# Kernel optimization log

Measured on AMD Instinct MI355X. Metric: run time of the kernel, lower is better.

The kernel has to match this reference:

```python
import jax, jax.numpy as jnp
import numpy as np

N, C, H, W = 4, 256, 64, 64
E = C // 2  # embed_dim = max(C//2, 1)


def setup_inputs() -> dict:
    key = jax.random.key(0)
    k1, k2, k3, k4 = jax.random.split(key, 4)
    x = jax.random.normal(k1, (N, C, H, W), dtype=jnp.float32)
    # 1x1 conv weights == channel-mixing matrices (bias=False), std=0.01 init
    W_theta = jax.random.normal(k2, (E, C), dtype=jnp.float32) * 0.01
    W_phi = jax.random.normal(k3, (E, C), dtype=jnp.float32) * 0.01
    W_proj = jax.random.normal(k4, (C, C), dtype=jnp.float32) * 0.01  # zero_init=False
    return {"x": x, "W_theta": W_theta, "W_phi": W_phi, "W_proj": W_proj}


def reference(x, W_theta, W_phi, W_proj):
    n, c, h, w = x.shape
    s = h * w
    xf = x.reshape(n, c, s)                      # [N, C, S]
    theta = jnp.einsum('ec,ncs->nes', W_theta, xf)  # [N, E, S]
    phi = jnp.einsum('ec,ncs->nes', W_phi, xf)      # [N, E, S]
    # f = theta^T @ phi, scaled by sqrt(embed_dim) (theta.shape[-1] after permute)
    scale = jnp.sqrt(jnp.asarray(theta.shape[1], dtype=x.dtype))
    f = jnp.einsum('nes,net->nst', theta, phi) / scale  # [N, S, S]
    f = jax.nn.softmax(f, axis=-1)
    # y = f @ g^T with g = x (unembedded values)
    y = jnp.einsum('nst,nct->ncs', f, xf)        # [N, C, S]
    residual = jnp.einsum('oc,ncs->nos', W_proj, y).reshape(n, c, h, w)
    return x + residual
```

## Files before the change

### kernel.cpp

```cpp
#include <hip/hip_runtime.h>
#include <cmath>

#define C_DIM 256
#define E_DIM 128
#define S_DIM 4096

typedef __bf16 bf16x8 __attribute__((ext_vector_type(8)));
typedef float  f32x4  __attribute__((ext_vector_type(4)));
typedef short  s16x8  __attribute__((ext_vector_type(8)));
typedef short  s16x4  __attribute__((ext_vector_type(4)));

__device__ __forceinline__ unsigned short f2bf(float f) {
  union { float f; unsigned u; } v; v.f = f;
  unsigned r = v.u + 0x7FFFu + ((v.u >> 16) & 1u);
  return (unsigned short)(r >> 16);
}
__device__ __forceinline__ unsigned short f2bf_tr(float f) {
  union { float f; unsigned u; } v; v.f = f;
  return (unsigned short)(v.u >> 16);
}
__device__ __forceinline__ bf16x8 as_bf(s16x8 v) {
  union { s16x8 s; bf16x8 b; } u; u.s = v; return u.b;
}
__device__ __forceinline__ bf16x8 f2b8(f32x4 v) { union { f32x4 f; bf16x8 b; } u; u.f = v; return u.b; }
__device__ __forceinline__ f32x4 b2f8(bf16x8 v) { union { bf16x8 b; f32x4 f; } u; u.b = v; return u.f; }
__device__ __forceinline__ f32x4 s2f8(s16x8 v)  { union { s16x8 s; f32x4 f; } u; u.s = v; return u.f; }
__device__ __forceinline__ s16x8 f2s8(f32x4 v)  { union { f32x4 f; s16x8 s; } u; u.f = v; return u.s; }

__global__ __launch_bounds__(256) void cast_w_kernel(
    const float* __restrict__ Wth, const float* __restrict__ Wph,
    const float* __restrict__ Wpr, short* __restrict__ Wb) {
  int t = blockIdx.x * 256 + threadIdx.x;
  int i = t * 4;
  const float* src; int j;
  if (i < 32768)      { src = Wth; j = i; }
  else if (i < 65536) { src = Wph; j = i - 32768; }
  else                { src = Wpr; j = i - 65536; }
  float4 v = *(const float4*)(src + j);
  s16x4 o;
  o[0] = (short)f2bf(v.x); o[1] = (short)f2bf(v.y);
  o[2] = (short)f2bf(v.z); o[3] = (short)f2bf(v.w);
  *(s16x4*)(Wb + i) = o;
}

__global__ __launch_bounds__(256) void mix_kernel(
    const float* __restrict__ x, const short* __restrict__ Wb,
    short* __restrict__ Qg, short* __restrict__ Kg, short* __restrict__ Xb,
    float qscale) {
  __shared__ short lxT[32 * C_DIM];
  int bid = blockIdx.x;
  int n = bid >> 7, s0 = (bid & 127) * 32;
  int tid = threadIdx.x;
  int wid = tid >> 6, lane = tid & 63, l15 = lane & 15, l4 = lane >> 4;

  {
    int cp = tid >> 1, su = tid & 1;
    const float* r0 = x + ((size_t)n * C_DIM + 2 * cp) * S_DIM + s0 + su * 16;
    const float* r1 = r0 + S_DIM;
    float a0[16], a1[16];
    #pragma unroll
    for (int j = 0; j < 4; ++j) {
      *(float4*)(a0 + 4 * j) = *(const float4*)(r0 + 4 * j);
      *(float4*)(a1 + 4 * j) = *(const float4*)(r1 + 4 * j);
    }
    short b0[16], b1[16];
    #pragma unroll
    for (int j = 0; j < 16; ++j) { b0[j] = (short)f2bf(a0[j]); b1[j] = (short)f2bf(a1[j]); }
    short* xb0 = Xb + ((size_t)n * C_DIM + 2 * cp) * S_DIM + s0 + su * 16;
    *(s16x8*)(xb0)             = *(s16x8*)(b0);
    *(s16x8*)(xb0 + 8)         = *(s16x8*)(b0 + 8);
    *(s16x8*)(xb0 + S_DIM)     = *(s16x8*)(b1);
    *(s16x8*)(xb0 + S_DIM + 8) = *(s16x8*)(b1 + 8);
    #pragma unroll
    for (int j = 0; j < 16; ++j) {
      int s = su * 16 + j;
      unsigned d = (unsigned)(unsigned short)b0[j] |
                   ((unsigned)(unsigned short)b1[j] << 16);
      *(unsigned*)((char*)lxT + s * 512 + ((4 * cp) ^ ((s & 7) << 4))) = d;
    }
  }
  __syncthreads();

  const short* Wq = Wb;
  const short* Wk = Wb + 32768;
  const f32x4 fzero = {0.f, 0.f, 0.f, 0.f};
  f32x4 accQ[2][2], accK[2][2];
  #pragma unroll
  for (int a = 0; a < 2; ++a)
    #pragma unroll
    for (int b = 0; b < 2; ++b) { accQ[a][b] = fzero; accK[a][b] = fzero; }

  #pragma unroll 2
  for (int kk = 0; kk < 8; ++kk) {
    bf16x8 bfr[2];
    #pragma unroll
    for (int nf = 0; nf < 2; ++nf) {
      int s = nf * 16 + l15;
      bfr[nf] = *(const bf16x8*)((char*)lxT + s * 512 +
                                 ((kk * 64 + l4 * 16) ^ ((s & 7) << 4)));
    }
    #pragma unroll
    for (int mf = 0; mf < 2; ++mf) {
      int e = wid * 32 + mf * 16 + l15;
      bf16x8 aq = *(const bf16x8*)(Wq + e * C_DIM + kk * 32 + l4 * 8);
      bf16x8 ak = *(const bf16x8*)(Wk + e * C_DIM + kk * 32 + l4 * 8);
      #pragma unroll
      for (int nf = 0; nf < 2; ++nf) {
        accQ[mf][nf] = __builtin_amdgcn_mfma_f32_16x16x32_bf16(aq, bfr[nf], accQ[mf][nf], 0, 0, 0);
        accK[mf][nf] = __builtin_amdgcn_mfma_f32_16x16x32_bf16(ak, bfr[nf], accK[mf][nf], 0, 0, 0);
      }
    }
  }

  #pragma unroll
  for (int mf = 0; mf < 2; ++mf) {
    #pragma unroll
    for (int nf = 0; nf < 2; ++nf) {
      int e = wid * 32 + mf * 16 + l4 * 4;
      int s = s0 + nf * 16 + l15;
      s16x4 pq, pk;
      #pragma unroll
      for (int r = 0; r < 4; ++r) {
        pq[r] = (short)f2bf(accQ[mf][nf][r] * qscale);
        pk[r] = (short)f2bf(accK[mf][nf][r]);
      }
      *(s16x4*)(Qg + ((size_t)n * S_DIM + s) * E_DIM + e) = pq;
      *(s16x4*)(Kg + ((size_t)n * S_DIM + s) * E_DIM + e) = pk;
    }
  }
}


#define QF(qs, ec) f2b8(RA[(qs) * 4 + (ec)])

#define QKT_BODY(KBUF)                                                        \
  {                                                                           \
    const char* kb = (const char*)lK + (KBUF) * 16384;                        \
    char* pw = (char*)lP + (KBUF) * 8192;                                     \
    RB[0] = fzero; RB[1] = fzero; RB[2] = fzero; RB[3] = fzero;               \
    int trow = tq * 16 + l15;                                                 \
    int swz = (trow & 7) << 4;                                                \
    __builtin_amdgcn_s_setprio(1);                                            \
    _Pragma("unroll")                                                         \
    for (int ec = 0; ec < 4; ++ec) {                                          \
      bf16x8 kf = *(const bf16x8*)(kb + trow * 256 + ((ec * 64 + l4 * 16) ^ swz)); \
      _Pragma("unroll")                                                       \
      for (int qs = 0; qs < 4; ++qs)                                          \
        RB[qs] = __builtin_amdgcn_mfma_f32_16x16x32_bf16(kf, QF(qs, ec), RB[qs], 0, 0, 0); \
    }                                                                         \
    __builtin_amdgcn_s_setprio(0);                                            \
    int tb2 = tq * 32 + l4 * 8;                                               \
    _Pragma("unroll")                                                         \
    for (int qs = 0; qs < 4; ++qs) {                                          \
      float p0 = __builtin_amdgcn_exp2f(RB[qs][0]);                           \
      float p1 = __builtin_amdgcn_exp2f(RB[qs][1]);                           \
      float p2 = __builtin_amdgcn_exp2f(RB[qs][2]);                           \
      float p3 = __builtin_amdgcn_exp2f(RB[qs][3]);                           \
      lsum[qs] += (p0 + p1) + (p2 + p3);                                      \
      uint2 dd;                                                               \
      dd.x = (unsigned)f2bf_tr(p0) | ((unsigned)f2bf_tr(p1) << 16);           \
      dd.y = (unsigned)f2bf_tr(p2) | ((unsigned)f2bf_tr(p3) << 16);           \
      int q = qs * 16 + l15;                                                  \
      *(uint2*)(pw + q * 128 + (tb2 ^ ((q & 7) << 4))) = dd;                  \
    }                                                                         \
  }

#define PV_VISSUE(OFF, TI)                                                    \
  _Pragma("unroll")                                                           \
  for (int kk = 0; kk < 2; ++kk)                                              \
    _Pragma("unroll")                                                         \
    for (int ct = 0; ct < 4; ++ct)                                            \
      RA[(OFF) + kk * 4 + ct] = s2f8(*(const s16x8*)(                         \
          Vb + (size_t)(cq * 64 + ct * 16 + l15) * S_DIM + (TI) * 64 + kk * 32 + l4 * 8));

#define PV_KCOMMIT(OFF, KBUFW)                                                \
  {                                                                           \
    char* kw = (char*)lK + (KBUFW) * 16384;                                   \
    _Pragma("unroll")                                                         \
    for (int jj = 0; jj < 4; ++jj) {                                          \
      int r = kr + 16 * jj;                                                   \
      *(s16x8*)(kw + r * 256 + ((kc * 16) ^ ((r & 7) << 4))) = f2s8(RB[(OFF) + jj]); \
    }                                                                         \
  }

#define PV_KLOAD(OFF, TI)                                                     \
  _Pragma("unroll")                                                           \
  for (int jj = 0; jj < 4; ++jj)                                              \
    RB[(OFF) + jj] = s2f8(*(const s16x8*)(                                    \
        Kb + (size_t)((TI) * 64 + kr + 16 * jj) * E_DIM + kc * 8));

#define PV_MFMA(OFF, PBUF)                                                    \
  {                                                                           \
    const char* pr = (const char*)lP + (PBUF) * 8192;                         \
    _Pragma("unroll")                                                         \
    for (int kk = 0; kk < 2; ++kk) {                                          \
      bf16x8 pf[4];                                                           \
      _Pragma("unroll")                                                       \
      for (int qs = 0; qs < 4; ++qs) {                                        \
        int q = qs * 16 + l15;                                                \
        pf[qs] = *(const bf16x8*)(pr + q * 128 + ((kk * 64 + l4 * 16) ^ ((q & 7) << 4))); \
      }                                                                       \
      __builtin_amdgcn_s_setprio(1);                                          \
      _Pragma("unroll")                                                       \
      for (int ct = 0; ct < 4; ++ct) {                                        \
        bf16x8 vf = as_bf(f2s8(RA[(OFF) + kk * 4 + ct]));                     \
        _Pragma("unroll")                                                     \
        for (int qs = 0; qs < 4; ++qs)                                        \
          acc[qs][ct] = __builtin_amdgcn_mfma_f32_16x16x32_bf16(pf[qs], vf, acc[qs][ct], 0, 0, 0); \
      }                                                                       \
      __builtin_amdgcn_s_setprio(0);                                          \
    }                                                                         \
  }

#define RAW_BARRIER()                                                         \
  asm volatile("s_waitcnt lgkmcnt(0)" ::: "memory");                          \
  __builtin_amdgcn_s_barrier();

__global__ __launch_bounds__(512, 2) void attn_kernel(
    const short* __restrict__ Qg, const short* __restrict__ Kg,
    const short* __restrict__ Xb, short* __restrict__ Yg) {
  __shared__ short lK[2 * 64 * E_DIM];
  __shared__ short lP[2 * 64 * 64];
  __shared__ float lsred[4 * 64];

  int bid = blockIdx.x;
  int xcd = bid & 7;
  int n   = xcd >> 1;
  int s0  = (((xcd & 1) << 5) + (bid >> 3)) * 64;

  int tid = threadIdx.x;
  int wid = tid >> 6, lane = tid & 63;
  int l15 = lane & 15, l4 = lane >> 4;

  const short* Kb = Kg + (size_t)n * S_DIM * E_DIM;
  const short* Vb = Xb + (size_t)n * (size_t)C_DIM * S_DIM;

  const f32x4 fzero = {0.f, 0.f, 0.f, 0.f};

  f32x4 RA[16];
  f32x4 RB[8];
  float lsum[4];
  f32x4 acc[4][4];

  int tq = wid;
  int cq = wid - 4;
  int idx = tid & 255;
  int kr = idx >> 4, kc = idx & 15;

  if (wid < 4) {
    #pragma unroll
    for (int qs = 0; qs < 4; ++qs) {
      const short* qp = Qg + ((size_t)n * S_DIM + s0 + qs * 16 + l15) * E_DIM + l4 * 8;
      #pragma unroll
      for (int ec = 0; ec < 4; ++ec) RA[qs * 4 + ec] = b2f8(*(const bf16x8*)(qp + ec * 32));
    }
    #pragma unroll
    for (int j = 0; j < 4; ++j) lsum[j] = 0.f;
  } else {
    #pragma unroll
    for (int a = 0; a < 4; ++a)
      #pragma unroll
      for (int b = 0; b < 4; ++b) acc[a][b] = fzero;
    PV_KLOAD(0, 0);
    PV_KCOMMIT(0, 0);
    PV_KLOAD(4, 1);
    PV_VISSUE(0, 0);
  }
  RAW_BARRIER();

  for (int j = 0; j < 32; ++j) {
    int i0 = 2 * j;
    if (wid < 4) {
      QKT_BODY(0);
    } else {
      if (j > 0)  PV_VISSUE(0, i0);
      PV_KCOMMIT(4, 1);
      if (j > 0)  PV_MFMA(8, 1);
      if (j < 31) PV_KLOAD(0, i0 + 2);
    }
    RAW_BARRIER();
    if (wid < 4) {
      QKT_BODY(1);
    } else {
      PV_VISSUE(8, i0 + 1);
      if (j < 31) PV_KCOMMIT(0, 0);
      PV_MFMA(0, 0);
      if (j < 31) PV_KLOAD(4, i0 + 3);
    }
    RAW_BARRIER();
  }
  if (wid >= 4) {
    PV_MFMA(8, 1);
  }

  if (wid < 4) {
    #pragma unroll
    for (int qs = 0; qs < 4; ++qs) {
      float v = lsum[qs];
      v += __shfl_xor(v, 16);
      v += __shfl_xor(v, 32);
      if (lane < 16) lsred[tq * 64 + qs * 16 + l15] = v;
    }
  }
  __syncthreads();

  short* yst = lK;
  if (wid >= 4) {
    #pragma unroll
    for (int qs = 0; qs < 4; ++qs) {
      #pragma unroll
      for (int r = 0; r < 4; ++r) {
        int q = qs * 16 + l4 * 4 + r;
        float tot = lsred[q] + lsred[64 + q] + lsred[128 + q] + lsred[192 + q];
        float rl = 1.0f / tot;
        #pragma unroll
        for (int ct = 0; ct < 4; ++ct) {
          int c = cq * 64 + ct * 16 + l15;
          *(unsigned short*)((char*)yst + q * 512 + ((c * 2) ^ ((q & 7) << 4))) =
              f2bf_tr(acc[qs][ct][r] * rl);
        }
      }
    }
  }
  __syncthreads();

  int rr = tid >> 3, chb = tid & 7;
  #pragma unroll
  for (int it = 0; it < 4; ++it) {
    int ch = chb + 8 * it;
    s16x8 v = *(const s16x8*)((char*)yst + rr * 512 + ((ch * 16) ^ ((rr & 7) << 4)));
    *(s16x8*)(Yg + ((size_t)n * S_DIM + s0 + rr) * C_DIM + ch * 8) = v;
  }
}

__global__ __launch_bounds__(256) void proj_kernel(
    const short* __restrict__ Yg, const short* __restrict__ Wpb,
    const float* __restrict__ x, float* __restrict__ out) {
  int bid = blockIdx.x;
  int n = bid >> 7, s0 = (bid & 127) * 32;
  int tid = threadIdx.x;
  int wid = tid >> 6, lane = tid & 63, l15 = lane & 15, l4 = lane >> 4;

  const f32x4 fzero = {0.f, 0.f, 0.f, 0.f};
  f32x4 acc[2][4];
  #pragma unroll
  for (int a = 0; a < 2; ++a)
    #pragma unroll
    for (int b = 0; b < 4; ++b) acc[a][b] = fzero;

  const short* ybase = Yg + (size_t)n * S_DIM * C_DIM;

  #pragma unroll 2
  for (int kk = 0; kk < 8; ++kk) {
    bf16x8 af[2];
    #pragma unroll
    for (int mf = 0; mf < 2; ++mf)
      af[mf] = *(const bf16x8*)(ybase + (size_t)(s0 + mf * 16 + l15) * C_DIM +
                                kk * 32 + l4 * 8);
    #pragma unroll
    for (int nf = 0; nf < 4; ++nf) {
      int o = wid * 64 + nf * 16 + l15;
      bf16x8 bfr = *(const bf16x8*)(Wpb + o * C_DIM + kk * 32 + l4 * 8);
      #pragma unroll
      for (int mf = 0; mf < 2; ++mf)
        acc[mf][nf] = __builtin_amdgcn_mfma_f32_16x16x32_bf16(af[mf], bfr, acc[mf][nf], 0, 0, 0);
    }
  }

  #pragma unroll
  for (int mf = 0; mf < 2; ++mf) {
    #pragma unroll
    for (int nf = 0; nf < 4; ++nf) {
      int o = wid * 64 + nf * 16 + l15;
      size_t idx = ((size_t)n * C_DIM + o) * (size_t)S_DIM + s0 + mf * 16 + l4 * 4;
      float4 xv = *(const float4*)(x + idx);
      float4 r;
      r.x = xv.x + acc[mf][nf][0];
      r.y = xv.y + acc[mf][nf][1];
      r.z = xv.z + acc[mf][nf][2];
      r.w = xv.w + acc[mf][nf][3];
      *(float4*)(out + idx) = r;
    }
  }
}

extern "C" void kernel_launch(void* const* d_in, const int* in_sizes, int n_in,
                              void* d_out, int out_size, void* d_ws, size_t ws_size,
                              hipStream_t stream) {
  const float* x   = (const float*)d_in[0];
  const float* Wth = (const float*)d_in[1];
  const float* Wph = (const float*)d_in[2];
  const float* Wpr = (const float*)d_in[3];
  float* out = (float*)d_out;

  short* q_ws  = (short*)d_ws;
  short* k_ws  = q_ws  + (size_t)4 * S_DIM * E_DIM;
  short* xb_ws = k_ws  + (size_t)4 * S_DIM * E_DIM;
  short* y_ws  = xb_ws + (size_t)4 * C_DIM * S_DIM;
  short* wb_ws = y_ws  + (size_t)4 * S_DIM * C_DIM;

  float qscale = 1.4426950408889634f / sqrtf(128.0f);

  cast_w_kernel<<<128, 256, 0, stream>>>(Wth, Wph, Wpr, wb_ws);
  mix_kernel<<<512, 256, 0, stream>>>(x, wb_ws, q_ws, k_ws, xb_ws, qscale);
  attn_kernel<<<256, 512, 0, stream>>>(q_ws, k_ws, xb_ws, y_ws);
  proj_kernel<<<512, 256, 0, stream>>>(y_ws, wb_ws + 65536, x, out);
}
```

Baseline: 115.6 us.

## Split attention key range across two blocks and enlarge query tile to 128

```diff
diff --git a/kernel.cpp b/kernel.cpp
--- a/kernel.cpp
+++ b/kernel.cpp
@@ -18,6 +18,10 @@
 __device__ __forceinline__ unsigned short f2bf_tr(float f) {
   union { float f; unsigned u; } v; v.f = f;
   return (unsigned short)(v.u >> 16);
+}
+__device__ __forceinline__ float bf2f(unsigned short b) {
+  union { unsigned u; float f; } v; v.u = ((unsigned)b) << 16;
+  return v.f;
 }
 __device__ __forceinline__ bf16x8 as_bf(s16x8 v) {
   union { s16x8 s; bf16x8 b; } u; u.s = v; return u.b;
@@ -133,35 +137,44 @@
 
 #define QF(qs, ec) f2b8(RA[(qs) * 4 + (ec)])
 
-#define QKT_BODY(KBUF)                                                        \
+#define QKT_BODY(B)                                                           \
   {                                                                           \
-    const char* kb = (const char*)lK + (KBUF) * 16384;                        \
-    char* pw = (char*)lP + (KBUF) * 8192;                                     \
-    RB[0] = fzero; RB[1] = fzero; RB[2] = fzero; RB[3] = fzero;               \
-    int trow = tq * 16 + l15;                                                 \
-    int swz = (trow & 7) << 4;                                                \
+    const char* kb = lK + (B) * 16384;                                        \
+    char* pw = lP + (B) * 16384;                                              \
+    _Pragma("unroll")                                                         \
+    for (int z = 0; z < 8; ++z) RB[z] = fzero;                                \
+    int trow0 = th2 * 32 + l15;                                               \
+    int trow1 = trow0 + 16;                                                   \
+    int swz0 = (trow0 & 7) << 4, swz1 = (trow1 & 7) << 4;                     \
     __builtin_amdgcn_s_setprio(1);                                            \
     _Pragma("unroll")                                                         \
     for (int ec = 0; ec < 4; ++ec) {                                          \
-      bf16x8 kf = *(const bf16x8*)(kb + trow * 256 + ((ec * 64 + l4 * 16) ^ swz)); \
+      bf16x8 kf0 = *(const bf16x8*)(kb + trow0 * 256 + ((ec * 64 + l4 * 16) ^ swz0)); \
+      bf16x8 kf1 = *(const bf16x8*)(kb + trow1 * 256 + ((ec * 64 + l4 * 16) ^ swz1)); \
       _Pragma("unroll")                                                       \
-      for (int qs = 0; qs < 4; ++qs)                                          \
-        RB[qs] = __builtin_amdgcn_mfma_f32_16x16x32_bf16(kf, QF(qs, ec), RB[qs], 0, 0, 0); \
+      for (int qs = 0; qs < 4; ++qs) {                                        \
+        RB[qs]     = __builtin_amdgcn_mfma_f32_16x16x32_bf16(kf0, QF(qs, ec), RB[qs], 0, 0, 0);     \
+        RB[4 + qs] = __builtin_amdgcn_mfma_f32_16x16x32_bf16(kf1, QF(qs, ec), RB[4 + qs], 0, 0, 0); \
+      }                                                                       \
     }                                                                         \
     __builtin_amdgcn_s_setprio(0);                                            \
-    int tb2 = tq * 32 + l4 * 8;                                               \
-    _Pragma("unroll")                                                         \
-    for (int qs = 0; qs < 4; ++qs) {                                          \
-      float p0 = __builtin_amdgcn_exp2f(RB[qs][0]);                           \
-      float p1 = __builtin_amdgcn_exp2f(RB[qs][1]);                           \
-      float p2 = __builtin_amdgcn_exp2f(RB[qs][2]);                           \
-      float p3 = __builtin_amdgcn_exp2f(RB[qs][3]);                           \
-      lsum[qs] += (p0 + p1) + (p2 + p3);                                      \
-      uint2 dd;                                                               \
-      dd.x = (unsigned)f2bf_tr(p0) | ((unsigned)f2bf_tr(p1) << 16);           \
-      dd.y = (unsigned)f2bf_tr(p2) | ((unsigned)f2bf_tr(p3) << 16);           \
-      int q = qs * 16 + l15;                                                  \
-      *(uint2*)(pw + q * 128 + (tb2 ^ ((q & 7) << 4))) = dd;                  \
+    _Pragma("unroll")                                                         \
+    for (int tb = 0; tb < 2; ++tb) {                                          \
+      int tbyte = th2 * 64 + tb * 32 + l4 * 8;                                \
+      _Pragma("unroll")                                                       \
+      for (int qs = 0; qs < 4; ++qs) {                                        \
+        f32x4 sv = RB[tb * 4 + qs];                                           \
+        float p0 = __builtin_amdgcn_exp2f(sv[0]);                             \
+        float p1 = __builtin_amdgcn_exp2f(sv[1]);                             \
+        float p2 = __builtin_amdgcn_exp2f(sv[2]);                             \
+        float p3 = __builtin_amdgcn_exp2f(sv[3]);                             \
+        lsum[qs] += (p0 + p1) + (p2 + p3);                                    \
+        uint2 dd;                                                             \
+        dd.x = (unsigned)f2bf_tr(p0) | ((unsigned)f2bf_tr(p1) << 16);         \
+        dd.y = (unsigned)f2bf_tr(p2) | ((unsigned)f2bf_tr(p3) << 16);         \
+        int q = qh * 64 + qs * 16 + l15;                                      \
+        *(uint2*)(pw + q * 128 + (tbyte ^ ((q & 7) << 4))) = dd;              \
+      }                                                                       \
     }                                                                         \
   }
 
@@ -171,11 +184,11 @@
     _Pragma("unroll")                                                         \
     for (int ct = 0; ct < 4; ++ct)                                            \
       RA[(OFF) + kk * 4 + ct] = s2f8(*(const s16x8*)(                         \
-          Vb + (size_t)(cq * 64 + ct * 16 + l15) * S_DIM + (TI) * 64 + kk * 32 + l4 * 8));
-
-#define PV_KCOMMIT(OFF, KBUFW)                                                \
+          Vb2 + (size_t)(cq * 64 + ct * 16 + l15) * S_DIM + (TI) * 64 + kk * 32 + l4 * 8));
+
+#define PV_KCOMMIT(OFF, B)                                                    \
   {                                                                           \
-    char* kw = (char*)lK + (KBUFW) * 16384;                                   \
+    char* kw = lK + (B) * 16384;                                              \
     _Pragma("unroll")                                                         \
     for (int jj = 0; jj < 4; ++jj) {                                          \
       int r = kr + 16 * jj;                                                   \
@@ -187,28 +200,32 @@
   _Pragma("unroll")                                                           \
   for (int jj = 0; jj < 4; ++jj)                                              \
     RB[(OFF) + jj] = s2f8(*(const s16x8*)(                                    \
-        Kb + (size_t)((TI) * 64 + kr + 16 * jj) * E_DIM + kc * 8));
+        Kb2 + (size_t)((TI) * 64 + kr + 16 * jj) * E_DIM + kc * 8));
 
 #define PV_MFMA(OFF, PBUF)                                                    \
   {                                                                           \
-    const char* pr = (const char*)lP + (PBUF) * 8192;                         \
+    const char* pr = lP + (PBUF) * 16384;                                     \
     _Pragma("unroll")                                                         \
     for (int kk = 0; kk < 2; ++kk) {                                          \
-      bf16x8 pf[4];                                                           \
       _Pragma("unroll")                                                       \
-      for (int qs = 0; qs < 4; ++qs) {                                        \
-        int q = qs * 16 + l15;                                                \
-        pf[qs] = *(const bf16x8*)(pr + q * 128 + ((kk * 64 + l4 * 16) ^ ((q & 7) << 4))); \
+      for (int qh2 = 0; qh2 < 2; ++qh2) {                                     \
+        bf16x8 pf[4];                                                         \
+        _Pragma("unroll")                                                     \
+        for (int qs = 0; qs < 4; ++qs) {                                      \
+          int q = qh2 * 64 + qs * 16 + l15;                                   \
+          pf[qs] = *(const bf16x8*)(pr + q * 128 + ((kk * 64 + l4 * 16) ^ ((q & 7) << 4))); \
+        }                                                                     \
+        __builtin_amdgcn_s_setprio(1);                                        \
+        _Pragma("unroll")                                                     \
+        for (int ct = 0; ct < 4; ++ct) {                                      \
+          bf16x8 vf = as_bf(f2s8(RA[(OFF) + kk * 4 + ct]));                   \
+          _Pragma("unroll")                                                   \
+          for (int qs = 0; qs < 4; ++qs)                                      \
+            acc[qh2 * 4 + qs][ct] = __builtin_amdgcn_mfma_f32_16x16x32_bf16(  \
+                pf[qs], vf, acc[qh2 * 4 + qs][ct], 0, 0, 0);                  \
+        }                                                                     \
+        __builtin_amdgcn_s_setprio(0);                                        \
       }                                                                       \
-      __builtin_amdgcn_s_setprio(1);                                          \
-      _Pragma("unroll")                                                       \
-      for (int ct = 0; ct < 4; ++ct) {                                        \
-        bf16x8 vf = as_bf(f2s8(RA[(OFF) + kk * 4 + ct]));                     \
-        _Pragma("unroll")                                                     \
-        for (int qs = 0; qs < 4; ++qs)                                        \
-          acc[qs][ct] = __builtin_amdgcn_mfma_f32_16x16x32_bf16(pf[qs], vf, acc[qs][ct], 0, 0, 0); \
-      }                                                                       \
-      __builtin_amdgcn_s_setprio(0);                                          \
     }                                                                         \
   }
 
@@ -218,39 +235,44 @@
 
 __global__ __launch_bounds__(512, 2) void attn_kernel(
     const short* __restrict__ Qg, const short* __restrict__ Kg,
-    const short* __restrict__ Xb, short* __restrict__ Yg) {
-  __shared__ short lK[2 * 64 * E_DIM];
-  __shared__ short lP[2 * 64 * 64];
-  __shared__ float lsred[4 * 64];
+    const short* __restrict__ Xb, short* __restrict__ Yn,
+    float* __restrict__ Ls) {
+  __shared__ __align__(16) char smem[66560];
+  char* lK = smem;
+  char* lP = smem + 32768;
+  float* lsred = (float*)(smem + 65536);
 
   int bid = blockIdx.x;
   int xcd = bid & 7;
   int n   = xcd >> 1;
-  int s0  = (((xcd & 1) << 5) + (bid >> 3)) * 64;
+  int th  = xcd & 1;
+  int s0  = (bid >> 3) * 128;
+  int tbase = th * 2048;
 
   int tid = threadIdx.x;
   int wid = tid >> 6, lane = tid & 63;
   int l15 = lane & 15, l4 = lane >> 4;
 
-  const short* Kb = Kg + (size_t)n * S_DIM * E_DIM;
-  const short* Vb = Xb + (size_t)n * (size_t)C_DIM * S_DIM;
+  const short* Kb2 = Kg + (size_t)n * S_DIM * E_DIM + (size_t)tbase * E_DIM;
+  const short* Vb2 = Xb + (size_t)n * (size_t)C_DIM * S_DIM + tbase;
 
   const f32x4 fzero = {0.f, 0.f, 0.f, 0.f};
 
   f32x4 RA[16];
   f32x4 RB[8];
   float lsum[4];
-  f32x4 acc[4][4];
-
-  int tq = wid;
-  int cq = wid - 4;
+  f32x4 acc[8][4];
+
+  int th2 = wid & 1;
+  int qh  = wid >> 1;
+  int cq  = wid - 4;
   int idx = tid & 255;
   int kr = idx >> 4, kc = idx & 15;
 
   if (wid < 4) {
     #pragma unroll
     for (int qs = 0; qs < 4; ++qs) {
-      const short* qp = Qg + ((size_t)n * S_DIM + s0 + qs * 16 + l15) * E_DIM + l4 * 8;
+      const short* qp = Qg + ((size_t)n * S_DIM + s0 + qh * 64 + qs * 16 + l15) * E_DIM + l4 * 8;
       #pragma unroll
       for (int ec = 0; ec < 4; ++ec) RA[qs * 4 + ec] = b2f8(*(const bf16x8*)(qp + ec * 32));
     }
@@ -258,7 +280,7 @@
     for (int j = 0; j < 4; ++j) lsum[j] = 0.f;
   } else {
     #pragma unroll
-    for (int a = 0; a < 4; ++a)
+    for (int a = 0; a < 8; ++a)
       #pragma unroll
       for (int b = 0; b < 4; ++b) acc[a][b] = fzero;
     PV_KLOAD(0, 0);
@@ -268,7 +290,7 @@
   }
   RAW_BARRIER();
 
-  for (int j = 0; j < 32; ++j) {
+  for (int j = 0; j < 16; ++j) {
     int i0 = 2 * j;
     if (wid < 4) {
       QKT_BODY(0);
@@ -276,16 +298,16 @@
       if (j > 0)  PV_VISSUE(0, i0);
       PV_KCOMMIT(4, 1);
       if (j > 0)  PV_MFMA(8, 1);
-      if (j < 31) PV_KLOAD(0, i0 + 2);
+      if (j < 15) PV_KLOAD(0, i0 + 2);
     }
     RAW_BARRIER();
     if (wid < 4) {
       QKT_BODY(1);
     } else {
       PV_VISSUE(8, i0 + 1);
-      if (j < 31) PV_KCOMMIT(0, 0);
+      if (j < 15) PV_KCOMMIT(0, 0);
       PV_MFMA(0, 0);
-      if (j < 31) PV_KLOAD(4, i0 + 3);
+      if (j < 15) PV_KLOAD(4, i0 + 3);
     }
     RAW_BARRIER();
   }
@@ -299,64 +321,87 @@
       float v = lsum[qs];
       v += __shfl_xor(v, 16);
       v += __shfl_xor(v, 32);
-      if (lane < 16) lsred[tq * 64 + qs * 16 + l15] = v;
+      if (lane < 16) lsred[th2 * 128 + qh * 64 + qs * 16 + l15] = v;
     }
   }
   __syncthreads();
 
-  short* yst = lK;
+  char* yst = smem;
   if (wid >= 4) {
     #pragma unroll
-    for (int qs = 0; qs < 4; ++qs) {
+    for (int qg = 0; qg < 8; ++qg) {
       #pragma unroll
       for (int r = 0; r < 4; ++r) {
-        int q = qs * 16 + l4 * 4 + r;
-        float tot = lsred[q] + lsred[64 + q] + lsred[128 + q] + lsred[192 + q];
-        float rl = 1.0f / tot;
+        int q = qg * 16 + l4 * 4 + r;
         #pragma unroll
         for (int ct = 0; ct < 4; ++ct) {
           int c = cq * 64 + ct * 16 + l15;
-          *(unsigned short*)((char*)yst + q * 512 + ((c * 2) ^ ((q & 7) << 4))) =
-              f2bf_tr(acc[qs][ct][r] * rl);
+          *(unsigned short*)(yst + q * 512 + ((c * 2) ^ ((q & 7) << 4))) =
+              f2bf_tr(acc[qg][ct][r]);
         }
       }
     }
   }
   __syncthreads();
 
-  int rr = tid >> 3, chb = tid & 7;
-  #pragma unroll
-  for (int it = 0; it < 4; ++it) {
-    int ch = chb + 8 * it;
-    s16x8 v = *(const s16x8*)((char*)yst + rr * 512 + ((ch * 16) ^ ((rr & 7) << 4)));
-    *(s16x8*)(Yg + ((size_t)n * S_DIM + s0 + rr) * C_DIM + ch * 8) = v;
+  size_t obase = ((size_t)th * 4 + n) * S_DIM;
+  #pragma unroll
+  for (int it = 0; it < 8; ++it) {
+    int ii = it * 512 + tid;
+    int rr = ii >> 5, ch = ii & 31;
+    s16x8 v = *(const s16x8*)(yst + rr * 512 + ((ch * 16) ^ ((rr & 7) << 4)));
+    *(s16x8*)(Yn + (obase + s0 + rr) * C_DIM + ch * 8) = v;
+  }
+  if (tid < 128) {
+    Ls[obase + s0 + tid] = lsred[tid] + lsred[128 + tid];
   }
 }
 
 __global__ __launch_bounds__(256) void proj_kernel(
-    const short* __restrict__ Yg, const short* __restrict__ Wpb,
-    const float* __restrict__ x, float* __restrict__ out) {
+    const short* __restrict__ Yn, const float* __restrict__ Ls,
+    const short* __restrict__ Wpb, const float* __restrict__ x,
+    float* __restrict__ out) {
   int bid = blockIdx.x;
   int n = bid >> 7, s0 = (bid & 127) * 32;
   int tid = threadIdx.x;
   int wid = tid >> 6, lane = tid & 63, l15 = lane & 15, l4 = lane >> 4;
 
+  const short* y0 = Yn + (size_t)n * S_DIM * C_DIM;
+  const short* y1 = y0 + (size_t)4 * S_DIM * C_DIM;
+  const float* l0 = Ls + (size_t)n * S_DIM;
+  const float* l1 = l0 + (size_t)4 * S_DIM;
+
+  int srow[2]; float rl[2];
+  #pragma unroll
+  for (int mf = 0; mf < 2; ++mf) {
+    int s = s0 + mf * 16 + l15;
+    srow[mf] = s;
+    rl[mf] = 1.0f / (l0[s] + l1[s]);
+  }
+
   const f32x4 fzero = {0.f, 0.f, 0.f, 0.f};
   f32x4 acc[2][4];
   #pragma unroll
   for (int a = 0; a < 2; ++a)
     #pragma unroll
     for (int b = 0; b < 4; ++b) acc[a][b] = fzero;
-
-  const short* ybase = Yg + (size_t)n * S_DIM * C_DIM;
 
   #pragma unroll 2
   for (int kk = 0; kk < 8; ++kk) {
     bf16x8 af[2];
     #pragma unroll
-    for (int mf = 0; mf < 2; ++mf)
-      af[mf] = *(const bf16x8*)(ybase + (size_t)(s0 + mf * 16 + l15) * C_DIM +
-                                kk * 32 + l4 * 8);
+    for (int mf = 0; mf < 2; ++mf) {
+      size_t off = (size_t)srow[mf] * C_DIM + kk * 32 + l4 * 8;
+      s16x8 a0 = *(const s16x8*)(y0 + off);
+      s16x8 a1 = *(const s16x8*)(y1 + off);
+      s16x8 t;
+      #pragma unroll
+      for (int jj = 0; jj < 8; ++jj) {
+        float f = (bf2f((unsigned short)a0[jj]) + bf2f((unsigned short)a1[jj])) * rl[mf];
+        t[jj] = (short)f2bf(f);
+      }
+      af[mf] = as_bf(t);
+    }
     #pragma unroll
     for (int nf = 0; nf < 4; ++nf) {
       int o = wid * 64 + nf * 16 + l15;
@@ -396,13 +441,14 @@
   short* q_ws  = (short*)d_ws;
   short* k_ws  = q_ws  + (size_t)4 * S_DIM * E_DIM;
   short* xb_ws = k_ws  + (size_t)4 * S_DIM * E_DIM;
-  short* y_ws  = xb_ws + (size_t)4 * C_DIM * S_DIM;
-  short* wb_ws = y_ws  + (size_t)4 * S_DIM * C_DIM;
+  short* yn_ws = xb_ws + (size_t)4 * C_DIM * S_DIM;
+  short* wb_ws = yn_ws + (size_t)2 * 4 * S_DIM * C_DIM;
+  float* ls_ws = (float*)(wb_ws + 131072);
 
   float qscale = 1.4426950408889634f / sqrtf(128.0f);
 
   cast_w_kernel<<<128, 256, 0, stream>>>(Wth, Wph, Wpr, wb_ws);
   mix_kernel<<<512, 256, 0, stream>>>(x, wb_ws, q_ws, k_ws, xb_ws, qscale);
-  attn_kernel<<<256, 512, 0, stream>>>(q_ws, k_ws, xb_ws, y_ws);
-  proj_kernel<<<512, 256, 0, stream>>>(y_ws, wb_ws + 65536, x, out);
-}
+  attn_kernel<<<256, 512, 0, stream>>>(q_ws, k_ws, xb_ws, yn_ws, ls_ws);
+  proj_kernel<<<512, 256, 0, stream>>>(yn_ws, ls_ws, wb_ws + 65536, x, out);
+}
```

Result: slower. 152.9 us (+32.3%).

## Load K tiles directly into QK^T wave registers, dropping LDS staging

Applied to the files above, without the earlier changes.

```diff
diff --git a/kernel.cpp b/kernel.cpp
--- a/kernel.cpp
+++ b/kernel.cpp
@@ -133,29 +133,32 @@
 
 #define QF(qs, ec) f2b8(RA[(qs) * 4 + (ec)])
 
-#define QKT_BODY(KBUF)                                                        \
+#define KF_ISSUE(OFF, TI)                                                     \
+  _Pragma("unroll")                                                           \
+  for (int ec = 0; ec < 4; ++ec)                                              \
+    RB[(OFF) + ec] = s2f8(*(const s16x8*)(                                    \
+        Kb + (size_t)((TI) * 64 + tq * 16 + l15) * E_DIM + ec * 32 + l4 * 8));
+
+#define QKT_BODY(B, KOFF)                                                     \
   {                                                                           \
-    const char* kb = (const char*)lK + (KBUF) * 16384;                        \
-    char* pw = (char*)lP + (KBUF) * 8192;                                     \
-    RB[0] = fzero; RB[1] = fzero; RB[2] = fzero; RB[3] = fzero;               \
-    int trow = tq * 16 + l15;                                                 \
-    int swz = (trow & 7) << 4;                                                \
+    char* pw = lP + (B) * 8192;                                               \
+    f32x4 sc[4] = {fzero, fzero, fzero, fzero};                               \
     __builtin_amdgcn_s_setprio(1);                                            \
     _Pragma("unroll")                                                         \
     for (int ec = 0; ec < 4; ++ec) {                                          \
-      bf16x8 kf = *(const bf16x8*)(kb + trow * 256 + ((ec * 64 + l4 * 16) ^ swz)); \
+      bf16x8 kf = f2b8(RB[(KOFF) + ec]);                                      \
       _Pragma("unroll")                                                       \
-      for (int qs = 0; qs < 4; ++qs)                                          \
-        RB[qs] = __builtin_amdgcn_mfma_f32_16x16x32_bf16(kf, QF(qs, ec), RB[qs], 0, 0, 0); \
+      for (int qs = 0; qs < 4; ++qs)                    \
+        sc[qs] = __builtin_amdgcn_mfma_f32_16x16x32_bf16(kf, QF(qs, ec), sc[qs], 0, 0, 0); \
     }                                                                         \
     __builtin_amdgcn_s_setprio(0);                                            \
     int tb2 = tq * 32 + l4 * 8;                                               \
     _Pragma("unroll")                                                         \
     for (int qs = 0; qs < 4; ++qs) {                                          \
-      float p0 = __builtin_amdgcn_exp2f(RB[qs][0]);                           \
-      float p1 = __builtin_amdgcn_exp2f(RB[qs][1]);                           \
-      float p2 = __builtin_amdgcn_exp2f(RB[qs][2]);                           \
-      float p3 = __builtin_amdgcn_exp2f(RB[qs][3]);                           \
+      float p0 = __builtin_amdgcn_exp2f(sc[qs][0]);                           \
+      float p1 = __builtin_amdgcn_exp2f(sc[qs][1]);                           \
+      float p2 = __builtin_amdgcn_exp2f(sc[qs][2]);                           \
+      float p3 = __builtin_amdgcn_exp2f(sc[qs][3]);                           \
       lsum[qs] += (p0 + p1) + (p2 + p3);                                      \
       uint2 dd;                                                               \
       dd.x = (unsigned)f2bf_tr(p0) | ((unsigned)f2bf_tr(p1) << 16);           \
@@ -173,25 +176,9 @@
       RA[(OFF) + kk * 4 + ct] = s2f8(*(const s16x8*)(                         \
           Vb + (size_t)(cq * 64 + ct * 16 + l15) * S_DIM + (TI) * 64 + kk * 32 + l4 * 8));
 
-#define PV_KCOMMIT(OFF, KBUFW)                                                \
-  {                                                                           \
-    char* kw = (char*)lK + (KBUFW) * 16384;                                   \
-    _Pragma("unroll")                                                         \
-    for (int jj = 0; jj < 4; ++jj) {                                          \
-      int r = kr + 16 * jj;                                                   \
-      *(s16x8*)(kw + r * 256 + ((kc * 16) ^ ((r & 7) << 4))) = f2s8(RB[(OFF) + jj]); \
-    }                                                                         \
-  }
-
-#define PV_KLOAD(OFF, TI)                                                     \
-  _Pragma("unroll")                                                           \
-  for (int jj = 0; jj < 4; ++jj)                                              \
-    RB[(OFF) + jj] = s2f8(*(const s16x8*)(                                    \
-        Kb + (size_t)((TI) * 64 + kr + 16 * jj) * E_DIM + kc * 8));
-
 #define PV_MFMA(OFF, PBUF)                                                    \
   {                                                                           \
-    const char* pr = (const char*)lP + (PBUF) * 8192;                         \
+    const char* pr = lP + (PBUF) * 8192;                                      \
     _Pragma("unroll")                                                         \
     for (int kk = 0; kk < 2; ++kk) {                                          \
       bf16x8 pf[4];                                                           \
@@ -219,9 +206,9 @@
 __global__ __launch_bounds__(512, 2) void attn_kernel(
     const short* __restrict__ Qg, const short* __restrict__ Kg,
     const short* __restrict__ Xb, short* __restrict__ Yg) {
-  __shared__ short lK[2 * 64 * E_DIM];
-  __shared__ short lP[2 * 64 * 64];
-  __shared__ float lsred[4 * 64];
+  __shared__ __align__(16) char smem[33792];
+  char* lP = smem;
+  float* lsred = (float*)(smem + 32768);
 
   int bid = blockIdx.x;
   int xcd = bid & 7;
@@ -244,8 +231,6 @@
 
   int tq = wid;
   int cq = wid - 4;
-  int idx = tid & 255;
-  int kr = idx >> 4, kc = idx & 15;
 
   if (wid < 4) {
     #pragma unroll
@@ -256,14 +241,13 @@
     }
     #pragma unroll
     for (int j = 0; j < 4; ++j) lsum[j] = 0.f;
+    KF_ISSUE(0, 0);
+    KF_ISSUE(4, 1);
   } else {
     #pragma unroll
     for (int a = 0; a < 4; ++a)
       #pragma unroll
       for (int b = 0; b < 4; ++b) acc[a][b] = fzero;
-    PV_KLOAD(0, 0);
-    PV_KCOMMIT(0, 0);
-    PV_KLOAD(4, 1);
     PV_VISSUE(0, 0);
   }
   RAW_BARRIER();
@@ -271,21 +255,19 @@
   for (int j = 0; j < 32; ++j) {
     int i0 = 2 * j;
     if (wid < 4) {
-      QKT_BODY(0);
+      QKT_BODY(0, 0);
+      if (j < 31) KF_ISSUE(0, i0 + 2);
     } else {
       if (j > 0)  PV_VISSUE(0, i0);
-      PV_KCOMMIT(4, 1);
       if (j > 0)  PV_MFMA(8, 1);
-      if (j < 31) PV_KLOAD(0, i0 + 2);
     }
     RAW_BARRIER();
     if (wid < 4) {
-      QKT_BODY(1);
+      QKT_BODY(1, 4);
+      if (j < 31) KF_ISSUE(4, i0 + 3);
     } else {
       PV_VISSUE(8, i0 + 1);
-      if (j < 31) PV_KCOMMIT(0, 0);
       PV_MFMA(0, 0);
-      if (j < 31) PV_KLOAD(4, i0 + 3);
     }
     RAW_BARRIER();
   }
@@ -304,7 +286,7 @@
   }
   __syncthreads();
 
-  short* yst = lK;
+  char* yst = smem;
   if (wid >= 4) {
     #pragma unroll
     for (int qs = 0; qs < 4; ++qs) {
@@ -316,7 +298,7 @@
         #pragma unroll
         for (int ct = 0; ct < 4; ++ct) {
           int c = cq * 64 + ct * 16 + l15;
-          *(unsigned short*)((char*)yst + q * 512 + ((c * 2) ^ ((q & 7) << 4))) =
+          *(unsigned short*)(yst + q * 512 + ((c * 2) ^ ((q & 7) << 4))) =
               f2bf_tr(acc[qs][ct][r] * rl);
         }
       }
@@ -328,7 +310,7 @@
   #pragma unroll
   for (int it = 0; it < 4; ++it) {
     int ch = chb + 8 * it;
-    s16x8 v = *(const s16x8*)((char*)yst + rr * 512 + ((ch * 16) ^ ((rr & 7) << 4)));
+    s16x8 v = *(const s16x8*)(yst + rr * 512 + ((ch * 16) ^ ((rr & 7) << 4)));
     *(s16x8*)(Yg + ((size_t)n * S_DIM + s0 + rr) * C_DIM + ch * 8) = v;
   }
 }
```

Result: slower. 138.5 us (+19.8%).

## Fuse output projection and residual add into attention kernel epilogue

Applied to the files above, without the earlier changes.

```diff
diff --git a/kernel.cpp b/kernel.cpp
--- a/kernel.cpp
+++ b/kernel.cpp
@@ -26,6 +26,8 @@
 __device__ __forceinline__ f32x4 b2f8(bf16x8 v) { union { bf16x8 b; f32x4 f; } u; u.b = v; return u.f; }
 __device__ __forceinline__ f32x4 s2f8(s16x8 v)  { union { s16x8 s; f32x4 f; } u; u.s = v; return u.f; }
 __device__ __forceinline__ s16x8 f2s8(f32x4 v)  { union { f32x4 f; s16x8 s; } u; u.f = v; return u.s; }
+
+#define MFMA16(a, b, c) __builtin_amdgcn_mfma_f32_16x16x32_bf16(a, b, c, 0, 0, 0)
 
 __global__ __launch_bounds__(256) void cast_w_kernel(
     const float* __restrict__ Wth, const float* __restrict__ Wph,
@@ -106,8 +108,8 @@
       bf16x8 ak = *(const bf16x8*)(Wk + e * C_DIM + kk * 32 + l4 * 8);
       #pragma unroll
       for (int nf = 0; nf < 2; ++nf) {
-        accQ[mf][nf] = __builtin_amdgcn_mfma_f32_16x16x32_bf16(aq, bfr[nf], accQ[mf][nf], 0, 0, 0);
-        accK[mf][nf] = __builtin_amdgcn_mfma_f32_16x16x32_bf16(ak, bfr[nf], accK[mf][nf], 0, 0, 0);
+        accQ[mf][nf] = MFMA16(aq, bfr[nf], accQ[mf][nf]);
+        accK[mf][nf] = MFMA16(ak, bfr[nf], accK[mf][nf]);
       }
     }
   }
@@ -133,10 +135,10 @@
 
 #define QF(qs, ec) f2b8(RA[(qs) * 4 + (ec)])
 
-#define QKT_BODY(KBUF)                                                        \
+#define QKT_BODY(B)                                                           \
   {                                                                           \
-    const char* kb = (const char*)lK + (KBUF) * 16384;                        \
-    char* pw = (char*)lP + (KBUF) * 8192;                                     \
+    const char* kb = (const char*)lK + (B) * 16384;                           \
+    char* pw = (char*)lP + (B) * 8192;                                        \
     RB[0] = fzero; RB[1] = fzero; RB[2] = fzero; RB[3] = fzero;               \
     int trow = tq * 16 + l15;                                                 \
     int swz = (trow & 7) << 4;                                                \
@@ -146,7 +148,7 @@
       bf16x8 kf = *(const bf16x8*)(kb + trow * 256 + ((ec * 64 + l4 * 16) ^ swz)); \
       _Pragma("unroll")                                                       \
       for (int qs = 0; qs < 4; ++qs)                                          \
-        RB[qs] = __builtin_amdgcn_mfma_f32_16x16x32_bf16(kf, QF(qs, ec), RB[qs], 0, 0, 0); \
+        RB[qs] = MFMA16(kf, QF(qs, ec), RB[qs]);                              \
     }                                                                         \
     __builtin_amdgcn_s_setprio(0);                                            \
     int tb2 = tq * 32 + l4 * 8;                                               \
@@ -173,9 +175,9 @@
       RA[(OFF) + kk * 4 + ct] = s2f8(*(const s16x8*)(                         \
           Vb + (size_t)(cq * 64 + ct * 16 + l15) * S_DIM + (TI) * 64 + kk * 32 + l4 * 8));
 
-#define PV_KCOMMIT(OFF, KBUFW)                                                \
+#define PV_KCOMMIT(OFF, B)                                                    \
   {                                                                           \
-    char* kw = (char*)lK + (KBUFW) * 16384;                                   \
+    char* kw = (char*)lK + (B) * 16384;                                       \
     _Pragma("unroll")                                                         \
     for (int jj = 0; jj < 4; ++jj) {                                          \
       int r = kr + 16 * jj;                                                   \
@@ -206,7 +208,7 @@
         bf16x8 vf = as_bf(f2s8(RA[(OFF) + kk * 4 + ct]));                     \
         _Pragma("unroll")                                                     \
         for (int qs = 0; qs < 4; ++qs)                                        \
-          acc[qs][ct] = __builtin_amdgcn_mfma_f32_16x16x32_bf16(pf[qs], vf, acc[qs][ct], 0, 0, 0); \
+          acc[qs][ct] = MFMA16(pf[qs], vf, acc[qs][ct]);                      \
       }                                                                       \
       __builtin_amdgcn_s_setprio(0);                                          \
     }                                                                         \
@@ -218,7 +220,8 @@
 
 __global__ __launch_bounds__(512, 2) void attn_kernel(
     const short* __restrict__ Qg, const short* __restrict__ Kg,
-    const short* __restrict__ Xb, short* __restrict__ Yg) {
+    const short* __restrict__ Xb, const short* __restrict__ Wpb,
+    const float* __restrict__ xg, float* __restrict__ out) {
   __shared__ short lK[2 * 64 * E_DIM];
   __shared__ short lP[2 * 64 * 64];
   __shared__ float lsred[4 * 64];
@@ -304,7 +307,7 @@
   }
   __syncthreads();
 
-  short* yst = lK;
+  char* yst = (char*)lK;
   if (wid >= 4) {
     #pragma unroll
     for (int qs = 0; qs < 4; ++qs) {
@@ -316,7 +319,7 @@
         #pragma unroll
         for (int ct = 0; ct < 4; ++ct) {
           int c = cq * 64 + ct * 16 + l15;
-          *(unsigned short*)((char*)yst + q * 512 + ((c * 2) ^ ((q & 7) << 4))) =
+          *(unsigned short*)(yst + q * 512 + ((c * 2) ^ ((q & 7) << 4))) =
               f2bf_tr(acc[qs][ct][r] * rl);
         }
       }
@@ -324,62 +327,45 @@
   }
   __syncthreads();
 
-  int rr = tid >> 3, chb = tid & 7;
-  #pragma unroll
-  for (int it = 0; it < 4; ++it) {
-    int ch = chb + 8 * it;
-    s16x8 v = *(const s16x8*)((char*)yst + rr * 512 + ((ch * 16) ^ ((rr & 7) << 4)));
-    *(s16x8*)(Yg + ((size_t)n * S_DIM + s0 + rr) * C_DIM + ch * 8) = v;
-  }
-}
-
-__global__ __launch_bounds__(256) void proj_kernel(
-    const short* __restrict__ Yg, const short* __restrict__ Wpb,
-    const float* __restrict__ x, float* __restrict__ out) {
-  int bid = blockIdx.x;
-  int n = bid >> 7, s0 = (bid & 127) * 32;
-  int tid = threadIdx.x;
-  int wid = tid >> 6, lane = tid & 63, l15 = lane & 15, l4 = lane >> 4;
-
-  const f32x4 fzero = {0.f, 0.f, 0.f, 0.f};
-  f32x4 acc[2][4];
-  #pragma unroll
-  for (int a = 0; a < 2; ++a)
-    #pragma unroll
-    for (int b = 0; b < 4; ++b) acc[a][b] = fzero;
-
-  const short* ybase = Yg + (size_t)n * S_DIM * C_DIM;
-
-  #pragma unroll 2
-  for (int kk = 0; kk < 8; ++kk) {
-    bf16x8 af[2];
-    #pragma unroll
-    for (int mf = 0; mf < 2; ++mf)
-      af[mf] = *(const bf16x8*)(ybase + (size_t)(s0 + mf * 16 + l15) * C_DIM +
-                                kk * 32 + l4 * 8);
-    #pragma unroll
-    for (int nf = 0; nf < 4; ++nf) {
-      int o = wid * 64 + nf * 16 + l15;
-      bf16x8 bfr = *(const bf16x8*)(Wpb + o * C_DIM + kk * 32 + l4 * 8);
-      #pragma unroll
-      for (int mf = 0; mf < 2; ++mf)
-        acc[mf][nf] = __builtin_amdgcn_mfma_f32_16x16x32_bf16(af[mf], bfr, acc[mf][nf], 0, 0, 0);
-    }
-  }
-
-  #pragma unroll
-  for (int mf = 0; mf < 2; ++mf) {
-    #pragma unroll
-    for (int nf = 0; nf < 4; ++nf) {
-      int o = wid * 64 + nf * 16 + l15;
-      size_t idx = ((size_t)n * C_DIM + o) * (size_t)S_DIM + s0 + mf * 16 + l4 * 4;
-      float4 xv = *(const float4*)(x + idx);
-      float4 r;
-      r.x = xv.x + acc[mf][nf][0];
-      r.y = xv.y + acc[mf][nf][1];
-      r.z = xv.z + acc[mf][nf][2];
-      r.w = xv.w + acc[mf][nf][3];
-      *(float4*)(out + idx) = r;
+  {
+    f32x4 pacc[4][2];
+    #pragma unroll
+    for (int a = 0; a < 4; ++a)
+      #pragma unroll
+      for (int b = 0; b < 2; ++b) pacc[a][b] = fzero;
+
+    #pragma unroll 2
+    for (int kk = 0; kk < 8; ++kk) {
+      bf16x8 af[4];
+      #pragma unroll
+      for (int mf = 0; mf < 4; ++mf) {
+        int q = mf * 16 + l15;
+        af[mf] = *(const bf16x8*)(yst + q * 512 + ((kk * 64 + l4 * 16) ^ ((q & 7) << 4)));
+      }
+      #pragma unroll
+      for (int nf = 0; nf < 2; ++nf) {
+        int o = wid * 32 + nf * 16 + l15;
+        bf16x8 bfr = *(const bf16x8*)(Wpb + o * C_DIM + kk * 32 + l4 * 8);
+        #pragma unroll
+        for (int mf = 0; mf < 4; ++mf)
+          pacc[mf][nf] = MFMA16(af[mf], bfr, pacc[mf][nf]);
+      }
+    }
+
+    #pragma unroll
+    for (int mf = 0; mf < 4; ++mf) {
+      #pragma unroll
+      for (int nf = 0; nf < 2; ++nf) {
+        int o = wid * 32 + nf * 16 + l15;
+        size_t idx2 = ((size_t)n * C_DIM + o) * (size_t)S_DIM + s0 + mf * 16 + l4 * 4;
+        float4 xv = *(const float4*)(xg + idx2);
+        float4 r;
+        r.x = xv.x + pacc[mf][nf][0];
+        r.y = xv.y + pacc[mf][nf][1];
+        r.z = xv.z + pacc[mf][nf][2];
+        r.w = xv.w + pacc[mf][nf][3];
+        *(float4*)(out + idx2) = r;
+      }
     }
   }
 }
@@ -396,13 +382,11 @@
   short* q_ws  = (short*)d_ws;
   short* k_ws  = q_ws  + (size_t)4 * S_DIM * E_DIM;
   short* xb_ws = k_ws  + (size_t)4 * S_DIM * E_DIM;
-  short* y_ws  = xb_ws + (size_t)4 * C_DIM * S_DIM;
-  short* wb_ws = y_ws  + (size_t)4 * S_DIM * C_DIM;
+  short* wb_ws = xb_ws + (size_t)4 * C_DIM * S_DIM;
 
   float qscale = 1.4426950408889634f / sqrtf(128.0f);
 
   cast_w_kernel<<<128, 256, 0, stream>>>(Wth, Wph, Wpr, wb_ws);
   mix_kernel<<<512, 256, 0, stream>>>(x, wb_ws, q_ws, k_ws, xb_ws, qscale);
-  attn_kernel<<<256, 512, 0, stream>>>(q_ws, k_ws, xb_ws, y_ws);
-  proj_kernel<<<512, 256, 0, stream>>>(y_ws, wb_ws + 65536, x, out);
-}
+  attn_kernel<<<256, 512, 0, stream>>>(q_ws, k_ws, xb_ws, wb_ws + 65536, x, out);
+}
```

After: 108.2 us. 1.07x faster.
